# Kernel tuning notes

Measured on AMD Instinct MI355X. Metric: run time of the kernel, lower is better.

Reference implementation:

```python
import jax, jax.numpy as jnp
import numpy as np

N_NODES = 100000


def gcn_conv(x, src, dst, norm, W, b):
    # PyG GCNConv: linear transform first, then normalized scatter-add aggregation, then bias.
    xw = x @ W                                   # [N, out]
    msgs = xw[src] * norm[:, None]               # [E+N, out] gathered, degree-normalized messages
    out = jax.ops.segment_sum(msgs, dst, num_segments=N_NODES)
    return out + b


def _build_graph(edge_index):
    # add self-loops (PyG gcn_norm default)
    loop = jnp.arange(N_NODES, dtype=edge_index.dtype)
    src = jnp.concatenate([edge_index[0], loop])
    dst = jnp.concatenate([edge_index[1], loop])
    deg = jax.ops.segment_sum(jnp.ones_like(dst, dtype=jnp.float32), dst, num_segments=N_NODES)
    dis = jnp.where(deg > 0, jax.lax.rsqrt(jnp.maximum(deg, 1.0)), 0.0)
    norm = dis[src] * dis[dst]                   # D^-1/2 (A+I) D^-1/2 edge weights
    return src, dst, norm


def setup_inputs() -> dict:
    key = jax.random.key(0)
    ks = jax.random.split(key, 6)
    F_IN, H, C, E = 128, 128, 8, 1600000
    x = jax.random.normal(ks[0], (N_NODES, F_IN), dtype=jnp.float32)
    edge_index = jax.random.randint(ks[1], (2, E), 0, N_NODES, dtype=jnp.int64)
    # glorot-style init for conv weights
    W1 = jax.random.normal(ks[2], (F_IN, H), dtype=jnp.float32) * (1.0 / np.sqrt(F_IN))
    b1 = jnp.zeros((H,), dtype=jnp.float32)
    W2 = jax.random.normal(ks[3], (H, C), dtype=jnp.float32) * (1.0 / np.sqrt(H))
    b2 = jnp.zeros((C,), dtype=jnp.float32)
    return {"x": x, "edge_index": edge_index, "W1": W1, "b1": b1, "W2": W2, "b2": b2}


def reference(x, edge_index, W1, b1, W2, b2):
    src, dst, norm = _build_graph(edge_index)
    h = gcn_conv(x, src, dst, norm, W1, b1)
    h = jax.nn.relu(h)
    # dropout is identity in eval mode
    out = gcn_conv(h, src, dst, norm, W2, b2)
    return jax.nn.log_softmax(out, axis=1)
```

## Files before the change

kernel.cpp:

```cpp
#include <hip/hip_runtime.h>

#define N_NODES 100000
#define NBKT 782
#define EPB 4096
#define BCAP 2560
#define SL_U 400000
#define Y2N (N_NODES * 8)

typedef unsigned int uint;
typedef unsigned short ushort;
typedef __attribute__((ext_vector_type(8))) short bf16x8;
typedef __attribute__((ext_vector_type(4))) float f32x4;
typedef __attribute__((ext_vector_type(2))) float f32x2;

union FragU { uint4 u; bf16x8 b; };

__device__ __forceinline__ uint pack_bf16_2(float a, float b) {
    uint ua = __float_as_uint(a), ub = __float_as_uint(b);
    ua += 0x7fff + ((ua >> 16) & 1);
    ub += 0x7fff + ((ub >> 16) & 1);
    return (ua >> 16) | (ub & 0xffff0000u);
}
__device__ __forceinline__ float bf_lo(uint u) { return __uint_as_float(u << 16); }
__device__ __forceinline__ float bf_hi(uint u) { return __uint_as_float(u & 0xffff0000u); }

__device__ __forceinline__ int edge_at(const int* __restrict__ ei, int idx, int is64) {
    return is64 ? ei[2 * idx] : ei[idx];
}

__global__ __launch_bounds__(256) void kZ(const int* __restrict__ ei,
                                          int* __restrict__ cursor,
                                          int* __restrict__ gflag) {
    __shared__ int shp;
    int t = threadIdx.x;
    int b = blockIdx.x;
    for (int i = b * 256 + t; i < NBKT; i += 1024) cursor[i] = 0;
    if (b == 0) {
        if (t == 0) shp = 0;
        __syncthreads();
        int any = 0;
        for (int j = t; j < 4096; j += 256) any |= ei[2 * j + 1];
        if (any) atomicOr(&shp, 1);
        __syncthreads();
        if (t == 0) gflag[0] = shp;
    }
}

__global__ __launch_bounds__(256) void kP(const int* __restrict__ ei, int E,
                                          const int* __restrict__ gflag,
                                          int* __restrict__ cursor,
                                          uint* __restrict__ bkt_data) {
    __shared__ int h[NBKT];
    __shared__ int base[NBKT];
    int t = threadIdx.x;
    int is64 = (gflag[0] == 0);
    for (int i = t; i < NBKT; i += 256) h[i] = 0;
    __syncthreads();
    int lo = blockIdx.x * EPB;
    int end = min(lo + EPB, E);
    for (int e = lo + t; e < end; e += 256) {
        int d = edge_at(ei, E + e, is64);
        atomicAdd(&h[d >> 7], 1);
    }
    __syncthreads();
    for (int i = t; i < NBKT; i += 256) {
        int c = h[i];
        base[i] = c ? atomicAdd(&cursor[i], c) : 0;
    }
    __syncthreads();
    for (int i = t; i < NBKT; i += 256) h[i] = 0;
    __syncthreads();
    for (int e = lo + t; e < end; e += 256) {
        int d = edge_at(ei, E + e, is64);
        int s = edge_at(ei, e, is64);
        int b = d >> 7;
        int r = atomicAdd(&h[b], 1);
        int pos = base[b] + r;
        if (pos < BCAP)
            bkt_data[(size_t)b * BCAP + pos] = ((uint)s << 7) | (uint)(d & 127);
    }
}

__global__ __launch_bounds__(256) void kB(const uint* __restrict__ bkt_data,
                                          const int* __restrict__ cursor,
                                          int* __restrict__ srcs,
                                          int* __restrict__ count,
                                          int* __restrict__ offs,
                                          float* __restrict__ dis) {
    __shared__ int lc[128];
    __shared__ int sc[128];
    __shared__ int lcur[128];
    int t = threadIdx.x;
    int b = blockIdx.x;
    if (t < 128) { lc[t] = 0; lcur[t] = 0; }
    __syncthreads();
    int start = b * BCAP;
    int n = min(cursor[b], BCAP);
    for (int i = t; i < n; i += 256)
        atomicAdd(&lc[bkt_data[start + i] & 127], 1);
    __syncthreads();
    if (t < 128) sc[t] = lc[t];
    __syncthreads();
    for (int d = 1; d < 128; d <<= 1) {
        int y = 0;
        if (t < 128 && t >= d) y = sc[t - d];
        __syncthreads();
        if (t < 128) sc[t] += y;
        __syncthreads();
    }
    if (t < 128) {
        int node = b * 128 + t;
        if (node < N_NODES) {
            int c = lc[t];
            count[node] = c;
            offs[node] = start + sc[t] - c;
            dis[node] = rsqrtf((float)c + 1.0f);
        }
    }
    __syncthreads();
    for (int i = t; i < n; i += 256) {
        uint rec = bkt_data[start + i];
        int dl = rec & 127;
        int r = atomicAdd(&lcur[dl], 1);
        srcs[start + (sc[dl] - lc[dl]) + r] = rec >> 7;
    }
}

__global__ __launch_bounds__(256) void k_gemm1(const float* __restrict__ x,
                                               const float* __restrict__ W,
                                               const float* __restrict__ dis,
                                               uint* __restrict__ y1s) {
    __shared__ uint4 WtA[2048];
    char* wt = (char*)WtA;
    int t = threadIdx.x;

    const float4* W4 = (const float4*)W;
#pragma unroll
    for (int ii = 0; ii < 4; ++ii) {
        int tile = t + 256 * ii;
        int nq = tile >> 5, kq = tile & 31;
        float4 r0 = W4[(4 * kq + 0) * 32 + nq];
        float4 r1 = W4[(4 * kq + 1) * 32 + nq];
        float4 r2 = W4[(4 * kq + 2) * 32 + nq];
        float4 r3 = W4[(4 * kq + 3) * 32 + nq];
        const float* p0 = (const float*)&r0;
        const float* p1 = (const float*)&r1;
        const float* p2 = (const float*)&r2;
        const float* p3 = (const float*)&r3;
#pragma unroll
        for (int cc = 0; cc < 4; ++cc) {
            int n = 4 * nq + cc;
            uint2 v;
            v.x = pack_bf16_2(p0[cc], p1[cc]);
            v.y = pack_bf16_2(p2[cc], p3[cc]);
            *(uint2*)(wt + n * 256 + (((kq >> 1) ^ (n & 7)) << 4) + ((kq & 1) << 3)) = v;
        }
    }
    __syncthreads();

    int w = t >> 6, lane = t & 63;
    int m = lane & 15, kg = lane >> 4;
    int row0 = blockIdx.x * 64 + 16 * w;

    int arow = row0 + m;
    bool av = arow < N_NODES;
    const float4* xr = (const float4*)(x + (size_t)arow * 128);
    float4 z4 = make_float4(0.f, 0.f, 0.f, 0.f);
    FragU af[4];
#pragma unroll
    for (int kf = 0; kf < 4; ++kf) {
        float4 g0 = av ? xr[8 * kf + 2 * kg]     : z4;
        float4 g1 = av ? xr[8 * kf + 2 * kg + 1] : z4;
        const float* a0 = (const float*)&g0;
        const float* a1 = (const float*)&g1;
        af[kf].u.x = pack_bf16_2(a0[0], a0[1]);
        af[kf].u.y = pack_bf16_2(a0[2], a0[3]);
        af[kf].u.z = pack_bf16_2(a1[0], a1[1]);
        af[kf].u.w = pack_bf16_2(a1[2], a1[3]);
    }

    int crow = row0 + 4 * kg;
    float dd[4];
#pragma unroll
    for (int rr = 0; rr < 4; ++rr)
        dd[rr] = (crow + rr < N_NODES) ? dis[crow + rr] : 0.0f;

    char* yb = (char*)y1s;
#pragma unroll
    for (int ct = 0; ct < 8; ++ct) {
        f32x4 acc = {0.f, 0.f, 0.f, 0.f};
#pragma unroll
        for (int kf = 0; kf < 4; ++kf) {
            int n = 16 * ct + m;
            bf16x8 bw = *(const bf16x8*)(wt + n * 256 + ((((kf << 2) | kg) ^ (n & 7)) << 4));
            acc = __builtin_amdgcn_mfma_f32_16x16x32_bf16(af[kf].b, bw, acc, 0, 0, 0);
        }
#pragma unroll
        for (int rr = 0; rr < 4; ++rr) {
            float v = acc[rr] * dd[rr];
            float p = __shfl_xor(v, 1, 64);
            if (!(lane & 1)) {
                int grow = crow + rr;
                if (grow < N_NODES) {
                    uint pk = __builtin_amdgcn_cvt_pk_fp8_f32(v, p, 0, false);
                    *(ushort*)(yb + (size_t)ct * (SL_U * 4) + grow * 16 + m) = (ushort)pk;
                }
            }
        }
    }
}

__global__ __launch_bounds__(256) void k_agg1s(const uint* __restrict__ y1s,
                                               const int* __restrict__ srcs,
                                               const int* __restrict__ offs,
                                               const int* __restrict__ count,
                                               const float* __restrict__ dis,
                                               const float* __restrict__ b1,
                                               const float* __restrict__ W2,
                                               float* __restrict__ y2p) {
    int t = threadIdx.x;
    int slice = blockIdx.x & 7;
    int nb = blockIdx.x >> 3;
    int g = t >> 3;
    int j = t & 7;
    int d = nb * 32 + g;

    float w0[8], w1[8];
    const float* wr0 = W2 + (size_t)(slice * 16 + 2 * j) * 8;
#pragma unroll
    for (int c = 0; c < 8; ++c) { w0[c] = wr0[c]; w1[c] = wr0[8 + c]; }

    const uint4* ybase = (const uint4*)(y1s + (size_t)slice * SL_U);
    f32x2 acc2[8];
#pragma unroll
    for (int c = 0; c < 8; ++c) acc2[c] = (f32x2){0.f, 0.f};

#define ACCUM_Q(q)                                                             \
    do {                                                                       \
        acc2[0] += __builtin_amdgcn_cvt_pk_f32_fp8((q).x, false);              \
        acc2[1] += __builtin_amdgcn_cvt_pk_f32_fp8((q).x, true);               \
        acc2[2] += __builtin_amdgcn_cvt_pk_f32_fp8((q).y, false);              \
        acc2[3] += __builtin_amdgcn_cvt_pk_f32_fp8((q).y, true);               \
        acc2[4] += __builtin_amdgcn_cvt_pk_f32_fp8((q).z, false);              \
        acc2[5] += __builtin_amdgcn_cvt_pk_f32_fp8((q).z, true);               \
        acc2[6] += __builtin_amdgcn_cvt_pk_f32_fp8((q).w, false);              \
        acc2[7] += __builtin_amdgcn_cvt_pk_f32_fp8((q).w, true);               \
    } while (0)

    int st = offs[d], n = count[d];
    int i = j;
    if (i <= n) {
        int sk = (i < n) ? srcs[st + i] : d;
        uint4 q = ybase[sk];
        for (i += 8; i <= n; i += 8) {
            int sk2 = (i < n) ? srcs[st + i] : d;
            uint4 qn = ybase[sk2];
            ACCUM_Q(q);
            q = qn;
        }
        ACCUM_Q(q);
    }
#undef ACCUM_Q

    float acc[16];
#pragma unroll
    for (int c = 0; c < 8; ++c) { acc[2 * c] = acc2[c][0]; acc[2 * c + 1] = acc2[c][1]; }

    int hi4 = (j >> 2) & 1, hi2 = (j >> 1) & 1, hi1 = j & 1;
    float v8[8];
#pragma unroll
    for (int c = 0; c < 8; ++c) {
        float keep = hi4 ? acc[c + 8] : acc[c];
        float send = hi4 ? acc[c] : acc[c + 8];
        v8[c] = keep + __shfl_xor(send, 4, 8);
    }
    float v4[4];
#pragma unroll
    for (int c = 0; c < 4; ++c) {
        float keep = hi2 ? v8[c + 4] : v8[c];
        float send = hi2 ? v8[c] : v8[c + 4];
        v4[c] = keep + __shfl_xor(send, 2, 8);
    }
    float v2[2];
#pragma unroll
    for (int c = 0; c < 2; ++c) {
        float keep = hi1 ? v4[c + 2] : v4[c];
        float send = hi1 ? v4[c] : v4[c + 2];
        v2[c] = keep + __shfl_xor(send, 1, 8);
    }

    float ddv = dis[d];
    float2 b = ((const float2*)b1)[slice * 8 + j];
    float h0 = fmaxf(fmaf(v2[0], ddv, b.x), 0.0f);
    float h1 = fmaxf(fmaf(v2[1], ddv, b.y), 0.0f);

    float p[8];
#pragma unroll
    for (int c = 0; c < 8; ++c) p[c] = h0 * w0[c] + h1 * w1[c];
    float q4[4];
#pragma unroll
    for (int c = 0; c < 4; ++c) {
        float keep = hi4 ? p[c + 4] : p[c];
        float send = hi4 ? p[c] : p[c + 4];
        q4[c] = keep + __shfl_xor(send, 4, 8);
    }
    float q2[2];
#pragma unroll
    for (int c = 0; c < 2; ++c) {
        float keep = hi2 ? q4[c + 2] : q4[c];
        float send = hi2 ? q4[c] : q4[c + 2];
        q2[c] = keep + __shfl_xor(send, 2, 8);
    }
    float keep = hi1 ? q2[1] : q2[0];
    float send = hi1 ? q2[0] : q2[1];
    float q = keep + __shfl_xor(send, 1, 8);

    y2p[(size_t)slice * Y2N + (size_t)d * 8 + j] = q * ddv;
}

__global__ __launch_bounds__(256) void k_pack(const float* __restrict__ y2p,
                                              uint4* __restrict__ y2b) {
    int i = blockIdx.x * 256 + threadIdx.x;
    if (i >= N_NODES) return;
    float4 a = make_float4(0.f, 0.f, 0.f, 0.f);
    float4 b = make_float4(0.f, 0.f, 0.f, 0.f);
#pragma unroll
    for (int s = 0; s < 8; ++s) {
        const float4* p = (const float4*)(y2p + (size_t)s * Y2N + (size_t)i * 8);
        float4 pa = p[0], pb = p[1];
        a.x += pa.x; a.y += pa.y; a.z += pa.z; a.w += pa.w;
        b.x += pb.x; b.y += pb.y; b.z += pb.z; b.w += pb.w;
    }
    uint4 o;
    o.x = pack_bf16_2(a.x, a.y);
    o.y = pack_bf16_2(a.z, a.w);
    o.z = pack_bf16_2(b.x, b.y);
    o.w = pack_bf16_2(b.z, b.w);
    y2b[i] = o;
}

__global__ __launch_bounds__(256) void k_agg2(const uint4* __restrict__ y2b,
                                              const int* __restrict__ srcs,
                                              const int* __restrict__ offs,
                                              const int* __restrict__ count,
                                              const float* __restrict__ dis,
                                              const float* __restrict__ b2,
                                              float* __restrict__ out) {
    int t = threadIdx.x;
    int g = (blockIdx.x * 256 + t) >> 3;
    int j = t & 7;
    if (g >= N_NODES) return;
    f32x2 acc2[4];
#pragma unroll
    for (int c = 0; c < 4; ++c) acc2[c] = (f32x2){0.f, 0.f};
    int st = offs[g], n = count[g];
    for (int i = j; i <= n; i += 8) {
        int sk = g;
        if (i < n) sk = srcs[st + i];
        uint4 q = y2b[sk];
        acc2[0] += (f32x2){bf_lo(q.x), bf_hi(q.x)};
        acc2[1] += (f32x2){bf_lo(q.y), bf_hi(q.y)};
        acc2[2] += (f32x2){bf_lo(q.z), bf_hi(q.z)};
        acc2[3] += (f32x2){bf_lo(q.w), bf_hi(q.w)};
    }
    float acc[8];
#pragma unroll
    for (int c = 0; c < 4; ++c) { acc[2 * c] = acc2[c][0]; acc[2 * c + 1] = acc2[c][1]; }

    int hi4 = (j >> 2) & 1, hi2 = (j >> 1) & 1, hi1 = j & 1;
    float v4[4];
#pragma unroll
    for (int c = 0; c < 4; ++c) {
        float keep = hi4 ? acc[c + 4] : acc[c];
        float send = hi4 ? acc[c] : acc[c + 4];
        v4[c] = keep + __shfl_xor(send, 4, 8);
    }
    float v2[2];
#pragma unroll
    for (int c = 0; c < 2; ++c) {
        float keep = hi2 ? v4[c + 2] : v4[c];
        float send = hi2 ? v4[c] : v4[c + 2];
        v2[c] = keep + __shfl_xor(send, 2, 8);
    }
    float keep = hi1 ? v2[1] : v2[0];
    float send = hi1 ? v2[0] : v2[1];
    float q = keep + __shfl_xor(send, 1, 8);

    float o = fmaf(q, dis[g], b2[j]);
    float m = o;
#pragma unroll
    for (int k = 1; k < 8; k <<= 1) m = fmaxf(m, __shfl_xor(m, k, 64));
    float e = expf(o - m);
    float ssum = e;
#pragma unroll
    for (int k = 1; k < 8; k <<= 1) ssum += __shfl_xor(ssum, k, 64);
    out[(size_t)g * 8 + j] = (o - m) - logf(ssum);
}

extern "C" void kernel_launch(void* const* d_in, const int* in_sizes, int n_in,
                              void* d_out, int out_size, void* d_ws, size_t ws_size,
                              hipStream_t stream) {
    const float* x  = (const float*)d_in[0];
    const int*   ei = (const int*)d_in[1];
    const float* W1 = (const float*)d_in[2];
    const float* b1 = (const float*)d_in[3];
    const float* W2 = (const float*)d_in[4];
    const float* b2 = (const float*)d_in[5];
    float* out = (float*)d_out;
    const int E = in_sizes[1] / 2;
    const int PB = (E + EPB - 1) / EPB;
    const size_t PADN = (size_t)NBKT * BCAP;

    int*   cursor   = (int*)d_ws;
    int*   gflag    = cursor + 784;
    int*   count    = gflag + 4;
    int*   offs     = count + N_NODES;
    float* dis      = (float*)(offs + N_NODES);
    uint*  bkt_data = (uint*)(dis + N_NODES);
    int*   srcs     = (int*)(bkt_data + PADN);
    uint*  y1s      = (uint*)(srcs + PADN);
    float* y2p      = (float*)(y1s + (size_t)8 * SL_U);
    uint4* y2b      = (uint4*)(y2p + (size_t)8 * Y2N);

    kZ     <<<4, 256, 0, stream>>>(ei, cursor, gflag);
    kP     <<<PB, 256, 0, stream>>>(ei, E, gflag, cursor, bkt_data);
    kB     <<<NBKT, 256, 0, stream>>>(bkt_data, cursor, srcs, count, offs, dis);

    k_gemm1<<<(N_NODES + 63) / 64, 256, 0, stream>>>(x, W1, dis, y1s);
    k_agg1s<<<8 * 3125, 256, 0, stream>>>(y1s, srcs, offs, count, dis, b1, W2, y2p);
    k_pack <<<(N_NODES + 255) / 256, 256, 0, stream>>>(y2p, y2b);
    k_agg2 <<<(N_NODES * 8 + 255) / 256, 256, 0, stream>>>(y2b, srcs, offs, count, dis, b2, out);
}
```

Measured before the change: 187.0 us.

## Halve feature slices in layer-1 aggregation, widening each gather to 32 bytes

The fp8 layer-1 features are re-laid out into 4 slices of 32 channels (32 bytes per node) instead of 8 slices of 16 channels. The aggregation kernel now gathers two uint4 per edge, so the srcs index reads are halved and the partial-sum buffer k_pack reduces shrinks by half. The price is more registers per thread (32 accumulators), fewer blocks, and the loss of the software-pipelined prefetch the old loop had.

```diff
diff --git a/kernel.cpp b/kernel.cpp
--- a/kernel.cpp
+++ b/kernel.cpp
@@ -4,7 +4,8 @@
 #define NBKT 782
 #define EPB 4096
 #define BCAP 2560
-#define SL_U 400000
+#define NSL 4
+#define SL_U 800000
 #define Y2N (N_NODES * 8)
 
 typedef unsigned int uint;
@@ -203,7 +204,8 @@
                 int grow = crow + rr;
                 if (grow < N_NODES) {
                     uint pk = __builtin_amdgcn_cvt_pk_fp8_f32(v, p, 0, false);
-                    *(ushort*)(yb + (size_t)ct * (SL_U * 4) + grow * 16 + m) = (ushort)pk;
+                    *(ushort*)(yb + (size_t)(ct >> 1) * (SL_U * 4)
+                               + (size_t)grow * 32 + (ct & 1) * 16 + m) = (ushort)pk;
                 }
             }
         }
@@ -219,84 +221,80 @@
                                                const float* __restrict__ W2,
                                                float* __restrict__ y2p) {
     int t = threadIdx.x;
-    int slice = blockIdx.x & 7;
-    int nb = blockIdx.x >> 3;
+    int slice = blockIdx.x & 3;
+    int nb = blockIdx.x >> 2;
     int g = t >> 3;
     int j = t & 7;
     int d = nb * 32 + g;
 
-    float w0[8], w1[8];
-    const float* wr0 = W2 + (size_t)(slice * 16 + 2 * j) * 8;
-#pragma unroll
-    for (int c = 0; c < 8; ++c) { w0[c] = wr0[c]; w1[c] = wr0[8 + c]; }
-
     const uint4* ybase = (const uint4*)(y1s + (size_t)slice * SL_U);
-    f32x2 acc2[8];
-#pragma unroll
-    for (int c = 0; c < 8; ++c) acc2[c] = (f32x2){0.f, 0.f};
-
-#define ACCUM_Q(q)                                                             \
-    do {                                                                       \
-        acc2[0] += __builtin_amdgcn_cvt_pk_f32_fp8((q).x, false);              \
-        acc2[1] += __builtin_amdgcn_cvt_pk_f32_fp8((q).x, true);               \
-        acc2[2] += __builtin_amdgcn_cvt_pk_f32_fp8((q).y, false);              \
-        acc2[3] += __builtin_amdgcn_cvt_pk_f32_fp8((q).y, true);               \
-        acc2[4] += __builtin_amdgcn_cvt_pk_f32_fp8((q).z, false);              \
-        acc2[5] += __builtin_amdgcn_cvt_pk_f32_fp8((q).z, true);               \
-        acc2[6] += __builtin_amdgcn_cvt_pk_f32_fp8((q).w, false);              \
-        acc2[7] += __builtin_amdgcn_cvt_pk_f32_fp8((q).w, true);               \
-    } while (0)
+    f32x2 acc2[16];
+#pragma unroll
+    for (int c = 0; c < 16; ++c) acc2[c] = (f32x2){0.f, 0.f};
 
     int st = offs[d], n = count[d];
-    int i = j;
-    if (i <= n) {
-        int sk = (i < n) ? srcs[st + i] : d;
-        uint4 q = ybase[sk];
-        for (i += 8; i <= n; i += 8) {
-            int sk2 = (i < n) ? srcs[st + i] : d;
-            uint4 qn = ybase[sk2];
-            ACCUM_Q(q);
-            q = qn;
-        }
-        ACCUM_Q(q);
-    }
-#undef ACCUM_Q
-
-    float acc[16];
-#pragma unroll
-    for (int c = 0; c < 8; ++c) { acc[2 * c] = acc2[c][0]; acc[2 * c + 1] = acc2[c][1]; }
+    for (int i = j; i <= n; i += 8) {
+        int sk = d;
+        if (i < n) sk = srcs[st + i];
+        uint4 q0 = ybase[(size_t)sk * 2];
+        uint4 q1 = ybase[(size_t)sk * 2 + 1];
+        acc2[0]  += __builtin_amdgcn_cvt_pk_f32_fp8(q0.x, false);
+        acc2[1]  += __builtin_amdgcn_cvt_pk_f32_fp8(q0.x, true);
+        acc2[2]  += __builtin_amdgcn_cvt_pk_f32_fp8(q0.y, false);
+        acc2[3]  += __builtin_amdgcn_cvt_pk_f32_fp8(q0.y, true);
+        acc2[4]  += __builtin_amdgcn_cvt_pk_f32_fp8(q0.z, false);
+        acc2[5]  += __builtin_amdgcn_cvt_pk_f32_fp8(q0.z, true);
+        acc2[6]  += __builtin_amdgcn_cvt_pk_f32_fp8(q0.w, false);
+        acc2[7]  += __builtin_amdgcn_cvt_pk_f32_fp8(q0.w, true);
+        acc2[8]  += __builtin_amdgcn_cvt_pk_f32_fp8(q1.x, false);
+        acc2[9]  += __builtin_amdgcn_cvt_pk_f32_fp8(q1.x, true);
+        acc2[10] += __builtin_amdgcn_cvt_pk_f32_fp8(q1.y, false);
+        acc2[11] += __builtin_amdgcn_cvt_pk_f32_fp8(q1.y, true);
+        acc2[12] += __builtin_amdgcn_cvt_pk_f32_fp8(q1.z, false);
+        acc2[13] += __builtin_amdgcn_cvt_pk_f32_fp8(q1.z, true);
+        acc2[14] += __builtin_amdgcn_cvt_pk_f32_fp8(q1.w, false);
+        acc2[15] += __builtin_amdgcn_cvt_pk_f32_fp8(q1.w, true);
+    }
+
+    float acc[32];
+#pragma unroll
+    for (int c = 0; c < 16; ++c) { acc[2 * c] = acc2[c][0]; acc[2 * c + 1] = acc2[c][1]; }
 
     int hi4 = (j >> 2) & 1, hi2 = (j >> 1) & 1, hi1 = j & 1;
+    float v16[16];
+#pragma unroll
+    for (int c = 0; c < 16; ++c) {
+        float keep = hi4 ? acc[c + 16] : acc[c];
+        float send = hi4 ? acc[c] : acc[c + 16];
+        v16[c] = keep + __shfl_xor(send, 4, 8);
+    }
     float v8[8];
 #pragma unroll
     for (int c = 0; c < 8; ++c) {
-        float keep = hi4 ? acc[c + 8] : acc[c];
-        float send = hi4 ? acc[c] : acc[c + 8];
-        v8[c] = keep + __shfl_xor(send, 4, 8);
+        float keep = hi2 ? v16[c + 8] : v16[c];
+        float send = hi2 ? v16[c] : v16[c + 8];
+        v8[c] = keep + __shfl_xor(send, 2, 8);
     }
     float v4[4];
 #pragma unroll
     for (int c = 0; c < 4; ++c) {
-        float keep = hi2 ? v8[c + 4] : v8[c];
-        float send = hi2 ? v8[c] : v8[c + 4];
-        v4[c] = keep + __shfl_xor(send, 2, 8);
-    }
-    float v2[2];
-#pragma unroll
-    for (int c = 0; c < 2; ++c) {
-        float keep = hi1 ? v4[c + 2] : v4[c];
-        float send = hi1 ? v4[c] : v4[c + 2];
-        v2[c] = keep + __shfl_xor(send, 1, 8);
+        float keep = hi1 ? v8[c + 4] : v8[c];
+        float send = hi1 ? v8[c] : v8[c + 4];
+        v4[c] = keep + __shfl_xor(send, 1, 8);
     }
 
     float ddv = dis[d];
-    float2 b = ((const float2*)b1)[slice * 8 + j];
-    float h0 = fmaxf(fmaf(v2[0], ddv, b.x), 0.0f);
-    float h1 = fmaxf(fmaf(v2[1], ddv, b.y), 0.0f);
-
+    float4 bv = ((const float4*)b1)[slice * 8 + j];
+    float h0 = fmaxf(fmaf(v4[0], ddv, bv.x), 0.0f);
+    float h1 = fmaxf(fmaf(v4[1], ddv, bv.y), 0.0f);
+    float h2 = fmaxf(fmaf(v4[2], ddv, bv.z), 0.0f);
+    float h3 = fmaxf(fmaf(v4[3], ddv, bv.w), 0.0f);
+
+    const float* wr = W2 + (size_t)(slice * 32 + 4 * j) * 8;
     float p[8];
 #pragma unroll
-    for (int c = 0; c < 8; ++c) p[c] = h0 * w0[c] + h1 * w1[c];
+    for (int c = 0; c < 8; ++c)
+        p[c] = h0 * wr[c] + h1 * wr[8 + c] + h2 * wr[16 + c] + h3 * wr[24 + c];
     float q4[4];
 #pragma unroll
     for (int c = 0; c < 4; ++c) {
@@ -325,7 +323,7 @@
     float4 a = make_float4(0.f, 0.f, 0.f, 0.f);
     float4 b = make_float4(0.f, 0.f, 0.f, 0.f);
 #pragma unroll
-    for (int s = 0; s < 8; ++s) {
+    for (int s = 0; s < NSL; ++s) {
         const float4* p = (const float4*)(y2p + (size_t)s * Y2N + (size_t)i * 8);
         float4 pa = p[0], pb = p[1];
         a.x += pa.x; a.y += pa.y; a.z += pa.z; a.w += pa.w;
@@ -419,15 +417,15 @@
     uint*  bkt_data = (uint*)(dis + N_NODES);
     int*   srcs     = (int*)(bkt_data + PADN);
     uint*  y1s      = (uint*)(srcs + PADN);
-    float* y2p      = (float*)(y1s + (size_t)8 * SL_U);
-    uint4* y2b      = (uint4*)(y2p + (size_t)8 * Y2N);
+    float* y2p      = (float*)(y1s + (size_t)NSL * SL_U);
+    uint4* y2b      = (uint4*)(y2p + (size_t)NSL * Y2N);
 
     kZ     <<<4, 256, 0, stream>>>(ei, cursor, gflag);
     kP     <<<PB, 256, 0, stream>>>(ei, E, gflag, cursor, bkt_data);
     kB     <<<NBKT, 256, 0, stream>>>(bkt_data, cursor, srcs, count, offs, dis);
 
     k_gemm1<<<(N_NODES + 63) / 64, 256, 0, stream>>>(x, W1, dis, y1s);
-    k_agg1s<<<8 * 3125, 256, 0, stream>>>(y1s, srcs, offs, count, dis, b1, W2, y2p);
+    k_agg1s<<<NSL * 3125, 256, 0, stream>>>(y1s, srcs, offs, count, dis, b1, W2, y2p);
     k_pack <<<(N_NODES + 255) / 256, 256, 0, stream>>>(y2p, y2b);
     k_agg2 <<<(N_NODES * 8 + 255) / 256, 256, 0, stream>>>(y2b, srcs, offs, count, dis, b2, out);
 }
```

After: 194.4 us. 1.04x slower.
